# Performance work log

Hardware: AMD Instinct MI355X
Metric: run time of the kernel (lower is better)

## Reference

```python
import jax, jax.numpy as jnp
import numpy as np

H = 16
D_MODEL = 1024
D_K = D_MODEL // H  # 64
TEMP = float(np.sqrt(D_K))


def setup_inputs() -> dict:
    key = jax.random.key(0)
    ks = jax.random.split(key, 12)
    N = 2048
    s_in = 1.0 / np.sqrt(D_MODEL)
    inp = {
        "query": jax.random.normal(ks[0], (N, D_MODEL), jnp.float32),
        "key": jax.random.normal(ks[1], (N, D_MODEL), jnp.float32),
        "value": jax.random.normal(ks[2], (N, D_MODEL), jnp.float32),
        "Wq": jax.random.normal(ks[3], (D_MODEL, D_MODEL), jnp.float32) * s_in,
        "bq": jnp.zeros((D_MODEL,), jnp.float32),
        "Wk": jax.random.normal(ks[4], (D_MODEL, D_MODEL), jnp.float32) * s_in,
        "bk": jnp.zeros((D_MODEL,), jnp.float32),
        "Wv": jax.random.normal(ks[5], (D_MODEL, D_MODEL), jnp.float32) * s_in,
        "bv": jnp.zeros((D_MODEL,), jnp.float32),
        "Wo": jax.random.normal(ks[6], (D_MODEL, D_MODEL), jnp.float32) * s_in,
        "bo": jnp.zeros((D_MODEL,), jnp.float32),
    }
    return inp


def reference(query, key, value, Wq, bq, Wk, bk, Wv, bv, Wo, bo):
    # Project then split heads exactly like view(-1, h, d_k).transpose(0, 1):
    # (N, d_model) -> (N, h, d_k) -> (h, N, d_k)
    q = (query @ Wq + bq).reshape(-1, H, D_K).transpose(1, 0, 2)
    k = (key @ Wk + bk).reshape(-1, H, D_K).transpose(1, 0, 2)
    v = (value @ Wv + bv).reshape(-1, H, D_K).transpose(1, 0, 2)
    # Scaled dot-product attention (dropout is inference-mode identity)
    scores = jnp.einsum("hnd,hmd->hnm", q / TEMP, k)  # (h, N, N)
    attn = jax.nn.softmax(scores, axis=-1)
    x = jnp.einsum("hnm,hmd->hnd", attn, v)  # (h, N, d_k)
    x = x.transpose(1, 0, 2).reshape(-1, H * D_K)  # (N, d_model)
    out = x @ Wo + bo
    return (out, attn)
```

## Files before the change

kernel.cpp:

```cpp
#include <hip/hip_runtime.h>
#include <math.h>

#define NTOK 2048
#define DMODEL 1024
#define NHEAD 16
#define DHEAD 64
#define NCH_S 4
#define NCH_A 2
#define TIL_S (NTOK / 64 / NCH_S)
#define TIL_A (NTOK / 64 / NCH_A)

typedef _Float16 f16x8 __attribute__((ext_vector_type(8)));
typedef _Float16 f16x4 __attribute__((ext_vector_type(4)));
typedef _Float16 f16x2 __attribute__((ext_vector_type(2)));
typedef float f32x4 __attribute__((ext_vector_type(4)));
typedef float f32x16 __attribute__((ext_vector_type(16)));

union U32H2 { f16x2 h; unsigned u; };
union U8 { f16x8 v; unsigned u[4]; };

__device__ __forceinline__ void split16(float x, _Float16& hi, _Float16& lo) {
    hi = (_Float16)x;
    lo = (_Float16)(x - (float)hi);
}
__device__ __forceinline__ unsigned packh(_Float16 a, _Float16 b) {
    U32H2 c; c.h = f16x2{a, b}; return c.u;
}

__global__ void __launch_bounds__(256) prep_w_kernel(
        const float* __restrict__ Wq, const float* __restrict__ Wk,
        const float* __restrict__ Wv, const float* __restrict__ Wo,
        _Float16* __restrict__ Wt) {
    __shared__ float T[32][33];
    const int z = blockIdx.z;
    const float* W = (z == 0) ? Wq : (z == 1) ? Wk : (z == 2) ? Wv : Wo;
    _Float16* Whi = Wt + (size_t)z * 2 * 1024 * 1024;
    _Float16* Wlo = Whi + (size_t)1024 * 1024;
    const int t = threadIdx.x;
    const int k0 = blockIdx.y * 32, n0 = blockIdx.x * 32;
    const int r = t >> 3, c4 = (t & 7) * 4;
    const float4 v = *(const float4*)(W + (size_t)(k0 + r) * DMODEL + n0 + c4);
    T[r][c4 + 0] = v.x; T[r][c4 + 1] = v.y; T[r][c4 + 2] = v.z; T[r][c4 + 3] = v.w;
    __syncthreads();
    f16x4 hv, lv;
#pragma unroll
    for (int j = 0; j < 4; ++j) {
        _Float16 h, l;
        split16(T[c4 + j][r], h, l);
        hv[j] = h; lv[j] = l;
    }
    *(f16x4*)(Whi + (size_t)(n0 + r) * DMODEL + k0 + c4) = hv;
    *(f16x4*)(Wlo + (size_t)(n0 + r) * DMODEL + k0 + c4) = lv;
}

__global__ void __launch_bounds__(256) prep_a_kernel(
        const float* __restrict__ q, const float* __restrict__ k, const float* __restrict__ v,
        _Float16* __restrict__ As) {
    const int z = blockIdx.y;
    const float* A = (z == 0) ? q : (z == 1) ? k : v;
    const size_t PL = (size_t)NTOK * DMODEL;
    _Float16* H = As + (size_t)z * 2 * PL;
    _Float16* L = H + PL;
    const size_t off = ((size_t)blockIdx.x * 256 + threadIdx.x) * 8;
    const float4 a = *(const float4*)(A + off);
    const float4 b = *(const float4*)(A + off + 4);
    f16x8 hv, lv; _Float16 h, lo;
    split16(a.x, h, lo); hv[0] = h; lv[0] = lo;
    split16(a.y, h, lo); hv[1] = h; lv[1] = lo;
    split16(a.z, h, lo); hv[2] = h; lv[2] = lo;
    split16(a.w, h, lo); hv[3] = h; lv[3] = lo;
    split16(b.x, h, lo); hv[4] = h; lv[4] = lo;
    split16(b.y, h, lo); hv[5] = h; lv[5] = lo;
    split16(b.z, h, lo); hv[6] = h; lv[6] = lo;
    split16(b.w, h, lo); hv[7] = h; lv[7] = lo;
    *(f16x8*)(H + off) = hv;
    *(f16x8*)(L + off) = lv;
}

__global__ void __launch_bounds__(256) qkv_mfma_kernel(
        const _Float16* __restrict__ As,
        const _Float16* __restrict__ Wt,
        const float* __restrict__ bq, const float* __restrict__ bk, const float* __restrict__ bv,
        _Float16* __restrict__ Qh, _Float16* __restrict__ Ql,
        _Float16* __restrict__ Kh, _Float16* __restrict__ Kl,
        _Float16* __restrict__ Vth, _Float16* __restrict__ Vtl) {
    __shared__ _Float16 Ah[64][40], Al[64][40], Bh[128][40], Bl[128][40];
    const int z = blockIdx.z;
    const size_t PL = (size_t)NTOK * DMODEL;
    const _Float16* AH = As + (size_t)z * 2 * PL;
    const _Float16* AL = AH + PL;
    const _Float16* WH = Wt + (size_t)z * 2 * 1024 * 1024;
    const _Float16* WL = WH + (size_t)1024 * 1024;
    const float* bias = (z == 0) ? bq : (z == 1) ? bk : bv;

    const int t = threadIdx.x;
    const int l = t & 63, wid = t >> 6;
    const int lr = l & 15, lk = l >> 4;
    const int m0 = blockIdx.y * 64, n0 = blockIdx.x * 128;
    const int wm = (wid >> 1) * 32, wn = (wid & 1) * 64;

    f32x4 acc[2][4];
#pragma unroll
    for (int mi = 0; mi < 2; ++mi)
#pragma unroll
        for (int ni = 0; ni < 4; ++ni)
#pragma unroll
            for (int e = 0; e < 4; ++e) acc[mi][ni][e] = 0.f;

    for (int k0 = 0; k0 < DMODEL; k0 += 32) {
        __syncthreads();
        {
            const int r = t >> 2, c8 = (t & 3) * 8;
            *(f16x8*)&Ah[r][c8] = *(const f16x8*)(AH + (size_t)(m0 + r) * DMODEL + k0 + c8);
            *(f16x8*)&Al[r][c8] = *(const f16x8*)(AL + (size_t)(m0 + r) * DMODEL + k0 + c8);
        }
#pragma unroll
        for (int p = 0; p < 2; ++p) {
            const int idx = t + p * 256;
            const int r = idx >> 2, c8 = (idx & 3) * 8;
            *(f16x8*)&Bh[r][c8] = *(const f16x8*)(WH + (size_t)(n0 + r) * DMODEL + k0 + c8);
            *(f16x8*)&Bl[r][c8] = *(const f16x8*)(WL + (size_t)(n0 + r) * DMODEL + k0 + c8);
        }
        __syncthreads();

        f16x8 ah[2], al[2], bh[4], bl[4];
#pragma unroll
        for (int i = 0; i < 2; ++i) {
            ah[i] = *(f16x8*)&Ah[wm + i * 16 + lr][lk * 8];
            al[i] = *(f16x8*)&Al[wm + i * 16 + lr][lk * 8];
        }
#pragma unroll
        for (int i = 0; i < 4; ++i) {
            bh[i] = *(f16x8*)&Bh[wn + i * 16 + lr][lk * 8];
            bl[i] = *(f16x8*)&Bl[wn + i * 16 + lr][lk * 8];
        }
        __builtin_amdgcn_s_setprio(1);
#pragma unroll
        for (int mi = 0; mi < 2; ++mi)
#pragma unroll
            for (int ni = 0; ni < 4; ++ni) {
                acc[mi][ni] = __builtin_amdgcn_mfma_f32_16x16x32_f16(ah[mi], bh[ni], acc[mi][ni], 0, 0, 0);
                acc[mi][ni] = __builtin_amdgcn_mfma_f32_16x16x32_f16(ah[mi], bl[ni], acc[mi][ni], 0, 0, 0);
                acc[mi][ni] = __builtin_amdgcn_mfma_f32_16x16x32_f16(al[mi], bh[ni], acc[mi][ni], 0, 0, 0);
            }
        __builtin_amdgcn_s_setprio(0);
    }

#pragma unroll
    for (int ni = 0; ni < 4; ++ni) {
        const int col = n0 + wn + ni * 16 + lr;
        const float bv_ = bias[col];
#pragma unroll
        for (int mi = 0; mi < 2; ++mi) {
            if (z == 2) {
                f16x4 hv, lv;
#pragma unroll
                for (int i = 0; i < 4; ++i) {
                    _Float16 h, lo;
                    split16(acc[mi][ni][i] + bv_, h, lo);
                    hv[i] = h; lv[i] = lo;
                }
                const int row = m0 + wm + mi * 16 + lk * 4;
                *(f16x4*)(Vth + (size_t)col * NTOK + row) = hv;
                *(f16x4*)(Vtl + (size_t)col * NTOK + row) = lv;
            } else {
#pragma unroll
                for (int i = 0; i < 4; ++i) {
                    const int row = m0 + wm + mi * 16 + lk * 4 + i;
                    float v = acc[mi][ni][i] + bv_;
                    if (z == 0) v *= 0.125f;
                    _Float16 h, lo;
                    split16(v, h, lo);
                    if (z == 0) { Qh[(size_t)row * DMODEL + col] = h; Ql[(size_t)row * DMODEL + col] = lo; }
                    else        { Kh[(size_t)row * DMODEL + col] = h; Kl[(size_t)row * DMODEL + col] = lo; }
                }
            }
        }
    }
}

__global__ void __launch_bounds__(256, 4) stats_kernel(
        const _Float16* __restrict__ Qh, const _Float16* __restrict__ Ql,
        const _Float16* __restrict__ Kh,
        float* __restrict__ lpart) {
    __shared__ _Float16 KB[2][64][64];
    const int t = threadIdx.x, l = t & 63, w = t >> 6, q = l & 31, h = l >> 5;
    const int hh = blockIdx.y, z = blockIdx.z;
    const int rw = blockIdx.x * 128 + w * 32;
    const int sr = t >> 3, sc = t & 7;

    f16x8 qbh[4], qbl[4];
#pragma unroll
    for (int s = 0; s < 4; ++s) {
        const size_t off = (size_t)(rw + q) * DMODEL + hh * DHEAD + s * 16 + h * 8;
        qbh[s] = *(const f16x8*)(Qh + off);
        qbl[s] = *(const f16x8*)(Ql + off);
    }

    float lsum = 0.f;
    {
        const int j0 = z * TIL_S * 64;
        const int r = sr, r2 = sr + 32;
        *(f16x8*)&KB[0][r][(sc ^ (r & 7)) * 8]   = *(const f16x8*)(Kh + (size_t)(j0 + r) * DMODEL + hh * DHEAD + sc * 8);
        *(f16x8*)&KB[0][r2][(sc ^ (r2 & 7)) * 8] = *(const f16x8*)(Kh + (size_t)(j0 + r2) * DMODEL + hh * DHEAD + sc * 8);
    }
    for (int it = 0; it < TIL_S; ++it) {
        __syncthreads();
        const int cur = it & 1;
        if (it + 1 < TIL_S) {
            const int j0 = (z * TIL_S + it + 1) * 64;
            const int r = sr, r2 = sr + 32;
            *(f16x8*)&KB[cur ^ 1][r][(sc ^ (r & 7)) * 8]   = *(const f16x8*)(Kh + (size_t)(j0 + r) * DMODEL + hh * DHEAD + sc * 8);
            *(f16x8*)&KB[cur ^ 1][r2][(sc ^ (r2 & 7)) * 8] = *(const f16x8*)(Kh + (size_t)(j0 + r2) * DMODEL + hh * DHEAD + sc * 8);
        }
#pragma unroll
        for (int kb = 0; kb < 2; ++kb) {
            f32x16 c;
#pragma unroll
            for (int r = 0; r < 16; ++r) c[r] = 0.f;
            __builtin_amdgcn_s_setprio(1);
#pragma unroll
            for (int s = 0; s < 4; ++s) {
                const int rk = kb * 32 + q; const int cc = ((2 * s + h) ^ (rk & 7)) * 8;
                const f16x8 ah = *(f16x8*)&KB[cur][rk][cc];
                c = __builtin_amdgcn_mfma_f32_32x32x16_f16(ah, qbh[s], c, 0, 0, 0);
                c = __builtin_amdgcn_mfma_f32_32x32x16_f16(ah, qbl[s], c, 0, 0, 0);
            }
            __builtin_amdgcn_s_setprio(0);
#pragma unroll
            for (int r = 0; r < 16; ++r) lsum += __expf(c[r]);
        }
    }
    lsum += __shfl_xor(lsum, 32);
    if (h == 0) lpart[((size_t)z * NHEAD + hh) * NTOK + rw + q] = lsum;
}

__global__ void __launch_bounds__(256, 4) attnpv_kernel(
        const _Float16* __restrict__ Qh, const _Float16* __restrict__ Ql,
        const _Float16* __restrict__ Kh, const _Float16* __restrict__ Vth,
        const float* __restrict__ lpart,
        float* __restrict__ attn, float* __restrict__ Xp0, float* __restrict__ Xp1) {
    __shared__ _Float16 KB[2][64][64];
    __shared__ _Float16 VB[2][64][64];
    const int t = threadIdx.x, l = t & 63, w = t >> 6, q = l & 31, h = l >> 5;
    const int hh = blockIdx.y, z = blockIdx.z;
    const int rw = blockIdx.x * 128 + w * 32;
    const int sr = t >> 3, sc = t & 7;
    const int qrow = rw + q;

    float lsum = 0.f;
#pragma unroll
    for (int zz = 0; zz < NCH_S; ++zz) lsum += lpart[((size_t)zz * NHEAD + hh) * NTOK + qrow];
    const float linv = 1.f / lsum;

    f16x8 qbh[4], qbl[4];
#pragma unroll
    for (int s = 0; s < 4; ++s) {
        const size_t off = (size_t)qrow * DMODEL + hh * DHEAD + s * 16 + h * 8;
        qbh[s] = *(const f16x8*)(Qh + off);
        qbl[s] = *(const f16x8*)(Ql + off);
    }

    f32x16 x0, x1;
#pragma unroll
    for (int r = 0; r < 16; ++r) { x0[r] = 0.f; x1[r] = 0.f; }

    auto stage = [&](int buf, int j0) {
#pragma unroll
        for (int p = 0; p < 2; ++p) {
            const int r = sr + p * 32; const int cs = (sc ^ (r & 7)) * 8;
            *(f16x8*)&KB[buf][r][cs] = *(const f16x8*)(Kh + (size_t)(j0 + r) * DMODEL + hh * DHEAD + sc * 8);
            *(f16x8*)&VB[buf][r][cs] = *(const f16x8*)(Vth + (size_t)(hh * DHEAD + r) * NTOK + j0 + sc * 8);
        }
    };
    stage(0, z * TIL_A * 64);

    for (int it = 0; it < TIL_A; ++it) {
        const int j0 = (z * TIL_A + it) * 64;
        __syncthreads();
        const int cur = it & 1;
        if (it + 1 < TIL_A) stage(cur ^ 1, (z * TIL_A + it + 1) * 64);

#pragma unroll
        for (int kb = 0; kb < 2; ++kb) {
            f32x16 c;
#pragma unroll
            for (int r = 0; r < 16; ++r) c[r] = 0.f;
            __builtin_amdgcn_s_setprio(1);
#pragma unroll
            for (int s = 0; s < 4; ++s) {
                const int rk = kb * 32 + q; const int cc = ((2 * s + h) ^ (rk & 7)) * 8;
                const f16x8 ah = *(f16x8*)&KB[cur][rk][cc];
                c = __builtin_amdgcn_mfma_f32_32x32x16_f16(ah, qbh[s], c, 0, 0, 0);
                c = __builtin_amdgcn_mfma_f32_32x32x16_f16(ah, qbl[s], c, 0, 0, 0);
            }
            __builtin_amdgcn_s_setprio(0);

            float p[16];
#pragma unroll
            for (int r = 0; r < 16; ++r) p[r] = __expf(c[r]) * linv;

            const int kbase = j0 + kb * 32;
#pragma unroll
            for (int i = 0; i < 4; ++i) {
                f32x4 st;
                st[0] = p[4 * i]; st[1] = p[4 * i + 1]; st[2] = p[4 * i + 2]; st[3] = p[4 * i + 3];
                *(f32x4*)(attn + ((size_t)hh * NTOK + qrow) * NTOK + kbase + 8 * i + 4 * h) = st;
            }

            _Float16 hf[16];
#pragma unroll
            for (int r = 0; r < 16; ++r) hf[r] = (_Float16)p[r];
            unsigned ph[8];
#pragma unroll
            for (int i = 0; i < 8; ++i) ph[i] = packh(hf[2 * i], hf[2 * i + 1]);

#pragma unroll
            for (int ss = 0; ss < 2; ++ss) {
                const int b = 4 * ss;
                const unsigned eh0 = __shfl_xor(h ? ph[b + 0] : ph[b + 2], 32);
                const unsigned eh1 = __shfl_xor(h ? ph[b + 1] : ph[b + 3], 32);
                U8 pah;
                pah.u[0] = h ? eh0 : ph[b + 0]; pah.u[1] = h ? eh1 : ph[b + 1];
                pah.u[2] = h ? ph[b + 2] : eh0; pah.u[3] = h ? ph[b + 3] : eh1;
                const int ks = kb * 2 + ss;
                __builtin_amdgcn_s_setprio(1);
                {
                    const int rd0 = q; const int cv0 = ((2 * ks + h) ^ (rd0 & 7)) * 8;
                    const f16x8 vh = *(f16x8*)&VB[cur][rd0][cv0];
                    x0 = __builtin_amdgcn_mfma_f32_32x32x16_f16(pah.v, vh, x0, 0, 0, 0);
                }
                {
                    const int rd1 = 32 + q; const int cv1 = ((2 * ks + h) ^ (rd1 & 7)) * 8;
                    const f16x8 vh = *(f16x8*)&VB[cur][rd1][cv1];
                    x1 = __builtin_amdgcn_mfma_f32_32x32x16_f16(pah.v, vh, x1, 0, 0, 0);
                }
                __builtin_amdgcn_s_setprio(0);
            }
        }
    }

    float* __restrict__ Xout = z ? Xp1 : Xp0;
#pragma unroll
    for (int r = 0; r < 16; ++r) {
        const int qloc = (r & 3) + 8 * (r >> 2) + 4 * h;
        Xout[(size_t)(rw + qloc) * DMODEL + hh * DHEAD + q]      = x0[r];
        Xout[(size_t)(rw + qloc) * DMODEL + hh * DHEAD + 32 + q] = x1[r];
    }
}

__global__ void __launch_bounds__(256) out_mfma_kernel(
        const float* __restrict__ Xp0, const float* __restrict__ Xp1,
        const _Float16* __restrict__ WH, const _Float16* __restrict__ WL,
        const float* __restrict__ bo, float* __restrict__ out) {
    __shared__ _Float16 Ah[64][40], Al[64][40], Bh[128][40], Bl[128][40];
    const int t = threadIdx.x;
    const int l = t & 63, wid = t >> 6;
    const int lr = l & 15, lk = l >> 4;
    const int m0 = blockIdx.y * 64, n0 = blockIdx.x * 128;
    const int wm = (wid >> 1) * 32, wn = (wid & 1) * 64;

    f32x4 acc[2][4];
#pragma unroll
    for (int mi = 0; mi < 2; ++mi)
#pragma unroll
        for (int ni = 0; ni < 4; ++ni)
#pragma unroll
            for (int e = 0; e < 4; ++e) acc[mi][ni][e] = 0.f;

    for (int k0 = 0; k0 < DMODEL; k0 += 32) {
        __syncthreads();
#pragma unroll
        for (int p = 0; p < 2; ++p) {
            const int idx = t + p * 256;
            const int r = idx >> 3, c4 = (idx & 7) * 4;
            const size_t off = (size_t)(m0 + r) * DMODEL + k0 + c4;
            const float4 v0 = *(const float4*)(Xp0 + off);
            const float4 v1 = *(const float4*)(Xp1 + off);
            f16x4 hv, lv; _Float16 h, lo;
            split16(v0.x + v1.x, h, lo); hv[0] = h; lv[0] = lo;
            split16(v0.y + v1.y, h, lo); hv[1] = h; lv[1] = lo;
            split16(v0.z + v1.z, h, lo); hv[2] = h; lv[2] = lo;
            split16(v0.w + v1.w, h, lo); hv[3] = h; lv[3] = lo;
            *(f16x4*)&Ah[r][c4] = hv;
            *(f16x4*)&Al[r][c4] = lv;
        }
#pragma unroll
        for (int p = 0; p < 2; ++p) {
            const int idx = t + p * 256;
            const int r = idx >> 2, c8 = (idx & 3) * 8;
            *(f16x8*)&Bh[r][c8] = *(const f16x8*)(WH + (size_t)(n0 + r) * DMODEL + k0 + c8);
            *(f16x8*)&Bl[r][c8] = *(const f16x8*)(WL + (size_t)(n0 + r) * DMODEL + k0 + c8);
        }
        __syncthreads();

        f16x8 ah[2], al[2], bh[4], bl[4];
#pragma unroll
        for (int i = 0; i < 2; ++i) {
            ah[i] = *(f16x8*)&Ah[wm + i * 16 + lr][lk * 8];
            al[i] = *(f16x8*)&Al[wm + i * 16 + lr][lk * 8];
        }
#pragma unroll
        for (int i = 0; i < 4; ++i) {
            bh[i] = *(f16x8*)&Bh[wn + i * 16 + lr][lk * 8];
            bl[i] = *(f16x8*)&Bl[wn + i * 16 + lr][lk * 8];
        }
        __builtin_amdgcn_s_setprio(1);
#pragma unroll
        for (int mi = 0; mi < 2; ++mi)
#pragma unroll
            for (int ni = 0; ni < 4; ++ni) {
                acc[mi][ni] = __builtin_amdgcn_mfma_f32_16x16x32_f16(ah[mi], bh[ni], acc[mi][ni], 0, 0, 0);
                acc[mi][ni] = __builtin_amdgcn_mfma_f32_16x16x32_f16(ah[mi], bl[ni], acc[mi][ni], 0, 0, 0);
                acc[mi][ni] = __builtin_amdgcn_mfma_f32_16x16x32_f16(al[mi], bh[ni], acc[mi][ni], 0, 0, 0);
            }
        __builtin_amdgcn_s_setprio(0);
    }

#pragma unroll
    for (int ni = 0; ni < 4; ++ni) {
        const int col = n0 + wn + ni * 16 + lr;
        const float bv_ = bo[col];
#pragma unroll
        for (int mi = 0; mi < 2; ++mi)
#pragma unroll
            for (int i = 0; i < 4; ++i) {
                const int row = m0 + wm + mi * 16 + lk * 4 + i;
                out[(size_t)row * DMODEL + col] = acc[mi][ni][i] + bv_;
            }
    }
}

extern "C" void kernel_launch(void* const* d_in, const int* in_sizes, int n_in,
                              void* d_out, int out_size, void* d_ws, size_t ws_size,
                              hipStream_t stream) {
    (void)in_sizes; (void)n_in; (void)out_size; (void)ws_size;
    const float* query = (const float*)d_in[0];
    const float* key_  = (const float*)d_in[1];
    const float* value = (const float*)d_in[2];
    const float* Wq = (const float*)d_in[3];
    const float* bq = (const float*)d_in[4];
    const float* Wk = (const float*)d_in[5];
    const float* bk = (const float*)d_in[6];
    const float* Wv = (const float*)d_in[7];
    const float* bv = (const float*)d_in[8];
    const float* Wo = (const float*)d_in[9];
    const float* bo = (const float*)d_in[10];

    float* out  = (float*)d_out;
    float* attn = out + (size_t)NTOK * DMODEL;

    const size_t MM = (size_t)1024 * 1024;
    _Float16* ws16 = (_Float16*)d_ws;
    _Float16* Wt  = ws16;
    _Float16* Qh  = ws16 + 8 * MM;
    _Float16* Ql  = Qh  + 2 * MM;
    _Float16* Kh_ = Ql  + 2 * MM;
    _Float16* Kl_ = Kh_ + 2 * MM;
    _Float16* Vth = Kl_ + 2 * MM;
    _Float16* Vtl = Vth + 2 * MM;

    float* Xp0   = (float*)ws16;
    float* lpart = (float*)(ws16 + 4 * MM);
    float* Xp1   = (float*)(ws16 + 20 * MM);

    _Float16* As = (_Float16*)attn;

    dim3 blk(256);
    prep_w_kernel<<<dim3(32, 32, 4), blk, 0, stream>>>(Wq, Wk, Wv, Wo, Wt);
    prep_a_kernel<<<dim3(1024, 3), blk, 0, stream>>>(query, key_, value, As);
    qkv_mfma_kernel<<<dim3(8, 32, 3), blk, 0, stream>>>(As, Wt, bq, bk, bv,
                                                        Qh, Ql, Kh_, Kl_, Vth, Vtl);
    stats_kernel<<<dim3(16, 16, NCH_S), blk, 0, stream>>>(Qh, Ql, Kh_, lpart);
    attnpv_kernel<<<dim3(16, 16, NCH_A), blk, 0, stream>>>(Qh, Ql, Kh_, Vth,
                                                           lpart, attn, Xp0, Xp1);
    out_mfma_kernel<<<dim3(8, 32), blk, 0, stream>>>(Xp0, Xp1, Wt + 6 * MM, Wt + 7 * MM, bo, out);
}
```

Measured before the change: 223.8 us.

## Fuse softmax stats and attention-PV kernels, drop key-split partials and unused low halves

The row-sum statistics kernel and the attention/PV kernel are merged into one kernel. Each block now makes two passes over all key tiles, which removes the key-dimension chunking, the lpart partial buffer and the two Xp partial outputs that the output GEMM had to add together. The QKV kernel also stops writing the unused low-precision halves of K and V. In exchange the attention grid shrinks to 256 blocks with a launch bound of 2 waves per SIMD. That cuts parallelism and latency hiding for the MFMA work and for the large attn-matrix store.

Measured after the change: 217.8 us. 2.7% less time.

```diff
diff --git a/kernel.cpp b/kernel.cpp
--- a/kernel.cpp
+++ b/kernel.cpp
@@ -5,10 +5,7 @@
 #define DMODEL 1024
 #define NHEAD 16
 #define DHEAD 64
-#define NCH_S 4
-#define NCH_A 2
-#define TIL_S (NTOK / 64 / NCH_S)
-#define TIL_A (NTOK / 64 / NCH_A)
+#define NTIL (NTOK / 64)
 
 typedef _Float16 f16x8 __attribute__((ext_vector_type(8)));
 typedef _Float16 f16x4 __attribute__((ext_vector_type(4)));
@@ -82,8 +79,7 @@
         const _Float16* __restrict__ Wt,
         const float* __restrict__ bq, const float* __restrict__ bk, const float* __restrict__ bv,
         _Float16* __restrict__ Qh, _Float16* __restrict__ Ql,
-        _Float16* __restrict__ Kh, _Float16* __restrict__ Kl,
-        _Float16* __restrict__ Vth, _Float16* __restrict__ Vtl) {
+        _Float16* __restrict__ Kh, _Float16* __restrict__ Vth) {
     __shared__ _Float16 Ah[64][40], Al[64][40], Bh[128][40], Bl[128][40];
     const int z = blockIdx.z;
     const size_t PL = (size_t)NTOK * DMODEL;
@@ -153,66 +149,73 @@
 #pragma unroll
         for (int mi = 0; mi < 2; ++mi) {
             if (z == 2) {
-                f16x4 hv, lv;
-#pragma unroll
-                for (int i = 0; i < 4; ++i) {
-                    _Float16 h, lo;
-                    split16(acc[mi][ni][i] + bv_, h, lo);
-                    hv[i] = h; lv[i] = lo;
-                }
+                f16x4 hv;
+#pragma unroll
+                for (int i = 0; i < 4; ++i) hv[i] = (_Float16)(acc[mi][ni][i] + bv_);
                 const int row = m0 + wm + mi * 16 + lk * 4;
                 *(f16x4*)(Vth + (size_t)col * NTOK + row) = hv;
-                *(f16x4*)(Vtl + (size_t)col * NTOK + row) = lv;
             } else {
 #pragma unroll
                 for (int i = 0; i < 4; ++i) {
                     const int row = m0 + wm + mi * 16 + lk * 4 + i;
                     float v = acc[mi][ni][i] + bv_;
-                    if (z == 0) v *= 0.125f;
-                    _Float16 h, lo;
-                    split16(v, h, lo);
-                    if (z == 0) { Qh[(size_t)row * DMODEL + col] = h; Ql[(size_t)row * DMODEL + col] = lo; }
-                    else        { Kh[(size_t)row * DMODEL + col] = h; Kl[(size_t)row * DMODEL + col] = lo; }
+                    if (z == 0) {
+                        v *= 0.125f;
+                        _Float16 h, lo;
+                        split16(v, h, lo);
+                        Qh[(size_t)row * DMODEL + col] = h;
+                        Ql[(size_t)row * DMODEL + col] = lo;
+                    } else {
+                        Kh[(size_t)row * DMODEL + col] = (_Float16)v;
+                    }
                 }
             }
         }
     }
 }
 
-__global__ void __launch_bounds__(256, 4) stats_kernel(
+__global__ void __launch_bounds__(256, 2) fused_attn_kernel(
         const _Float16* __restrict__ Qh, const _Float16* __restrict__ Ql,
-        const _Float16* __restrict__ Kh,
-        float* __restrict__ lpart) {
+        const _Float16* __restrict__ Kh, const _Float16* __restrict__ Vth,
+        float* __restrict__ attn, float* __restrict__ Xp) {
     __shared__ _Float16 KB[2][64][64];
+    __shared__ _Float16 VB[2][64][64];
     const int t = threadIdx.x, l = t & 63, w = t >> 6, q = l & 31, h = l >> 5;
-    const int hh = blockIdx.y, z = blockIdx.z;
+    const int hh = blockIdx.y;
     const int rw = blockIdx.x * 128 + w * 32;
     const int sr = t >> 3, sc = t & 7;
+    const int qrow = rw + q;
 
     f16x8 qbh[4], qbl[4];
 #pragma unroll
     for (int s = 0; s < 4; ++s) {
-        const size_t off = (size_t)(rw + q) * DMODEL + hh * DHEAD + s * 16 + h * 8;
+        const size_t off = (size_t)qrow * DMODEL + hh * DHEAD + s * 16 + h * 8;
         qbh[s] = *(const f16x8*)(Qh + off);
         qbl[s] = *(const f16x8*)(Ql + off);
     }
 
+    auto stageK = [&](int buf, int j0) {
+#pragma unroll
+        for (int p = 0; p < 2; ++p) {
+            const int r = sr + p * 32; const int cs = (sc ^ (r & 7)) * 8;
+            *(f16x8*)&KB[buf][r][cs] = *(const f16x8*)(Kh + (size_t)(j0 + r) * DMODEL + hh * DHEAD + sc * 8);
+        }
+    };
+    auto stageKV = [&](int buf, int j0) {
+#pragma unroll
+        for (int p = 0; p < 2; ++p) {
+            const int r = sr + p * 32; const int cs = (sc ^ (r & 7)) * 8;
+            *(f16x8*)&KB[buf][r][cs] = *(const f16x8*)(Kh + (size_t)(j0 + r) * DMODEL + hh * DHEAD + sc * 8);
+            *(f16x8*)&VB[buf][r][cs] = *(const f16x8*)(Vth + (size_t)(hh * DHEAD + r) * NTOK + j0 + sc * 8);
+        }
+    };
+
     float lsum = 0.f;
-    {
-        const int j0 = z * TIL_S * 64;
-        const int r = sr, r2 = sr + 32;
-        *(f16x8*)&KB[0][r][(sc ^ (r & 7)) * 8]   = *(const f16x8*)(Kh + (size_t)(j0 + r) * DMODEL + hh * DHEAD + sc * 8);
-        *(f16x8*)&KB[0][r2][(sc ^ (r2 & 7)) * 8] = *(const f16x8*)(Kh + (size_t)(j0 + r2) * DMODEL + hh * DHEAD + sc * 8);
-    }
-    for (int it = 0; it < TIL_S; ++it) {
+    stageK(0, 0);
+    for (int it = 0; it < NTIL; ++it) {
         __syncthreads();
         const int cur = it & 1;
-        if (it + 1 < TIL_S) {
-            const int j0 = (z * TIL_S + it + 1) * 64;
-            const int r = sr, r2 = sr + 32;
-            *(f16x8*)&KB[cur ^ 1][r][(sc ^ (r & 7)) * 8]   = *(const f16x8*)(Kh + (size_t)(j0 + r) * DMODEL + hh * DHEAD + sc * 8);
-            *(f16x8*)&KB[cur ^ 1][r2][(sc ^ (r2 & 7)) * 8] = *(const f16x8*)(Kh + (size_t)(j0 + r2) * DMODEL + hh * DHEAD + sc * 8);
-        }
+        if (it + 1 < NTIL) stageK(cur ^ 1, (it + 1) * 64);
 #pragma unroll
         for (int kb = 0; kb < 2; ++kb) {
             f32x16 c;
@@ -232,54 +235,19 @@
         }
     }
     lsum += __shfl_xor(lsum, 32);
-    if (h == 0) lpart[((size_t)z * NHEAD + hh) * NTOK + rw + q] = lsum;
-}
-
-__global__ void __launch_bounds__(256, 4) attnpv_kernel(
-        const _Float16* __restrict__ Qh, const _Float16* __restrict__ Ql,
-        const _Float16* __restrict__ Kh, const _Float16* __restrict__ Vth,
-        const float* __restrict__ lpart,
-        float* __restrict__ attn, float* __restrict__ Xp0, float* __restrict__ Xp1) {
-    __shared__ _Float16 KB[2][64][64];
-    __shared__ _Float16 VB[2][64][64];
-    const int t = threadIdx.x, l = t & 63, w = t >> 6, q = l & 31, h = l >> 5;
-    const int hh = blockIdx.y, z = blockIdx.z;
-    const int rw = blockIdx.x * 128 + w * 32;
-    const int sr = t >> 3, sc = t & 7;
-    const int qrow = rw + q;
-
-    float lsum = 0.f;
-#pragma unroll
-    for (int zz = 0; zz < NCH_S; ++zz) lsum += lpart[((size_t)zz * NHEAD + hh) * NTOK + qrow];
     const float linv = 1.f / lsum;
 
-    f16x8 qbh[4], qbl[4];
-#pragma unroll
-    for (int s = 0; s < 4; ++s) {
-        const size_t off = (size_t)qrow * DMODEL + hh * DHEAD + s * 16 + h * 8;
-        qbh[s] = *(const f16x8*)(Qh + off);
-        qbl[s] = *(const f16x8*)(Ql + off);
-    }
-
     f32x16 x0, x1;
 #pragma unroll
     for (int r = 0; r < 16; ++r) { x0[r] = 0.f; x1[r] = 0.f; }
 
-    auto stage = [&](int buf, int j0) {
-#pragma unroll
-        for (int p = 0; p < 2; ++p) {
-            const int r = sr + p * 32; const int cs = (sc ^ (r & 7)) * 8;
-            *(f16x8*)&KB[buf][r][cs] = *(const f16x8*)(Kh + (size_t)(j0 + r) * DMODEL + hh * DHEAD + sc * 8);
-            *(f16x8*)&VB[buf][r][cs] = *(const f16x8*)(Vth + (size_t)(hh * DHEAD + r) * NTOK + j0 + sc * 8);
-        }
-    };
-    stage(0, z * TIL_A * 64);
-
-    for (int it = 0; it < TIL_A; ++it) {
-        const int j0 = (z * TIL_A + it) * 64;
+    __syncthreads();
+    stageKV(0, 0);
+    for (int it = 0; it < NTIL; ++it) {
+        const int j0 = it * 64;
         __syncthreads();
         const int cur = it & 1;
-        if (it + 1 < TIL_A) stage(cur ^ 1, (z * TIL_A + it + 1) * 64);
+        if (it + 1 < NTIL) stageKV(cur ^ 1, (it + 1) * 64);
 
 #pragma unroll
         for (int kb = 0; kb < 2; ++kb) {
@@ -340,17 +308,16 @@
         }
     }
 
-    float* __restrict__ Xout = z ? Xp1 : Xp0;
 #pragma unroll
     for (int r = 0; r < 16; ++r) {
         const int qloc = (r & 3) + 8 * (r >> 2) + 4 * h;
-        Xout[(size_t)(rw + qloc) * DMODEL + hh * DHEAD + q]      = x0[r];
-        Xout[(size_t)(rw + qloc) * DMODEL + hh * DHEAD + 32 + q] = x1[r];
+        Xp[(size_t)(rw + qloc) * DMODEL + hh * DHEAD + q]      = x0[r];
+        Xp[(size_t)(rw + qloc) * DMODEL + hh * DHEAD + 32 + q] = x1[r];
     }
 }
 
 __global__ void __launch_bounds__(256) out_mfma_kernel(
-        const float* __restrict__ Xp0, const float* __restrict__ Xp1,
+        const float* __restrict__ Xp,
         const _Float16* __restrict__ WH, const _Float16* __restrict__ WL,
         const float* __restrict__ bo, float* __restrict__ out) {
     __shared__ _Float16 Ah[64][40], Al[64][40], Bh[128][40], Bl[128][40];
@@ -375,13 +342,12 @@
             const int idx = t + p * 256;
             const int r = idx >> 3, c4 = (idx & 7) * 4;
             const size_t off = (size_t)(m0 + r) * DMODEL + k0 + c4;
-            const float4 v0 = *(const float4*)(Xp0 + off);
-            const float4 v1 = *(const float4*)(Xp1 + off);
+            const float4 v0 = *(const float4*)(Xp + off);
             f16x4 hv, lv; _Float16 h, lo;
-            split16(v0.x + v1.x, h, lo); hv[0] = h; lv[0] = lo;
-            split16(v0.y + v1.y, h, lo); hv[1] = h; lv[1] = lo;
-            split16(v0.z + v1.z, h, lo); hv[2] = h; lv[2] = lo;
-            split16(v0.w + v1.w, h, lo); hv[3] = h; lv[3] = lo;
+            split16(v0.x, h, lo); hv[0] = h; lv[0] = lo;
+            split16(v0.y, h, lo); hv[1] = h; lv[1] = lo;
+            split16(v0.z, h, lo); hv[2] = h; lv[2] = lo;
+            split16(v0.w, h, lo); hv[3] = h; lv[3] = lo;
             *(f16x4*)&Ah[r][c4] = hv;
             *(f16x4*)&Al[r][c4] = lv;
         }
@@ -456,13 +422,9 @@
     _Float16* Qh  = ws16 + 8 * MM;
     _Float16* Ql  = Qh  + 2 * MM;
     _Float16* Kh_ = Ql  + 2 * MM;
-    _Float16* Kl_ = Kh_ + 2 * MM;
-    _Float16* Vth = Kl_ + 2 * MM;
-    _Float16* Vtl = Vth + 2 * MM;
-
-    float* Xp0   = (float*)ws16;
-    float* lpart = (float*)(ws16 + 4 * MM);
-    float* Xp1   = (float*)(ws16 + 20 * MM);
+    _Float16* Vth = Kh_ + 2 * MM;
+
+    float* Xp = (float*)ws16;
 
     _Float16* As = (_Float16*)attn;
 
@@ -470,9 +432,7 @@
     prep_w_kernel<<<dim3(32, 32, 4), blk, 0, stream>>>(Wq, Wk, Wv, Wo, Wt);
     prep_a_kernel<<<dim3(1024, 3), blk, 0, stream>>>(query, key_, value, As);
     qkv_mfma_kernel<<<dim3(8, 32, 3), blk, 0, stream>>>(As, Wt, bq, bk, bv,
-                                                        Qh, Ql, Kh_, Kl_, Vth, Vtl);
-    stats_kernel<<<dim3(16, 16, NCH_S), blk, 0, stream>>>(Qh, Ql, Kh_, lpart);
-    attnpv_kernel<<<dim3(16, 16, NCH_A), blk, 0, stream>>>(Qh, Ql, Kh_, Vth,
-                                                           lpart, attn, Xp0, Xp1);
-    out_mfma_kernel<<<dim3(8, 32), blk, 0, stream>>>(Xp0, Xp1, Wt + 6 * MM, Wt + 7 * MM, bo, out);
-}
+                                                        Qh, Ql, Kh_, Vth);
+    fused_attn_kernel<<<dim3(16, 16), blk, 0, stream>>>(Qh, Ql, Kh_, Vth, attn, Xp);
+    out_mfma_kernel<<<dim3(8, 32), blk, 0, stream>>>(Xp, Wt + 6 * MM, Wt + 7 * MM, bo, out);
+}
```
